# Performance work log

Hardware: AMD Instinct MI355X
Metric: run time of the kernel (lower is better)

Reference implementation:

```python
import jax, jax.numpy as jnp
import numpy as np

SLOPE = 10.0
NTR = 4.0
DTR = 0.0
DELTA = 3
MARG = 2


def _gt(x):
    return jax.nn.sigmoid(x * SLOPE)


def setup_inputs() -> dict:
    key = jax.random.key(0)
    x = jax.random.uniform(key, (16, 3, 512, 512), dtype=jnp.float32)
    return {"x": x}


def reference(x):
    B, C, H, W = x.shape
    d = DELTA
    # zero-pad H and W by delta (matches the two torch.cat calls)
    im_b = jnp.pad(x, ((0, 0), (0, 0), (d, d), (d, d)))

    roll_hw = lambda s: jnp.roll(im_b, s, axis=(2, 3))
    diff_11 = roll_hw((1, 1)) - im_b
    diff_nn11 = roll_hw((-1, -1)) - im_b
    diff_01 = roll_hw((0, 1)) - im_b
    diff_n01 = roll_hw((0, -1)) - im_b
    diff_10 = roll_hw((1, 0)) - im_b
    diff_n10 = roll_hw((-1, 0)) - im_b
    diff_n11 = roll_hw((-1, 1)) - im_b
    diff_1n1 = roll_hw((1, -1)) - im_b

    # NOTE: the original rolls the diff tensors over dims (1,2) = (channel, H).
    # We reproduce that exactly for faithfulness.
    rl = lambda t, s: jnp.roll(t, s, axis=(1, 2))

    ad_10 = jnp.abs(diff_10)
    ad_10 = ad_10 * _gt(ad_10 - DTR)
    e10a = _gt(ad_10 - jnp.abs(diff_01)) + _gt(ad_10 - jnp.abs(diff_n01)) + _gt(ad_10 - jnp.abs(diff_n10))
    # original repeats the roll(diff_01) term twice
    e10b = (_gt(ad_10 - jnp.abs(rl(diff_01, (1, 0))))
            + _gt(ad_10 - jnp.abs(rl(diff_n01, (1, 0))))
            + _gt(ad_10 - jnp.abs(rl(diff_01, (1, 0)))))
    g10 = _gt(e10a + e10b - NTR)
    e10 = g10 * _gt(diff_10)
    e10n = g10 * _gt(-diff_10)

    ad_01 = jnp.abs(diff_01)
    ad_01 = ad_01 * _gt(ad_10 - DTR)  # original uses ad_10 here (faithful)
    e01a = _gt(ad_01 - jnp.abs(diff_10)) + _gt(ad_01 - jnp.abs(diff_n10)) + _gt(ad_01 - jnp.abs(diff_n01))
    e01b = (_gt(ad_01 - jnp.abs(rl(diff_10, (0, 1))))
            + _gt(ad_01 - jnp.abs(rl(diff_n10, (0, 1))))
            + _gt(ad_01 - jnp.abs(rl(diff_01, (0, 1)))))
    g01 = _gt(e01a + e01b - NTR)
    e01 = g01 * _gt(diff_01)
    e01n = g01 * _gt(diff_01)  # original uses +diff_01 for both (faithful)

    ad_11 = jnp.abs(diff_11)
    ad_11 = ad_11 * _gt(ad_11 - DTR)
    e11a = _gt(ad_11 - jnp.abs(diff_n11)) + _gt(ad_11 - jnp.abs(diff_1n1)) + _gt(ad_11 - jnp.abs(diff_nn11))
    e11b = (_gt(ad_11 - jnp.abs(rl(diff_n11, (1, 1))))
            + _gt(ad_11 - jnp.abs(rl(diff_1n1, (1, 1))))
            + _gt(ad_11 - jnp.abs(rl(diff_11, (1, 1)))))
    g11 = _gt(e11a + e11b - NTR)
    e11 = g11 * _gt(diff_11)
    e11n = g11 * _gt(-diff_11)

    ad_n11 = jnp.abs(diff_n11)
    ad_n11 = ad_n11 * (ad_n11 > DTR).astype(x.dtype)  # hard threshold here (faithful)
    en11a = _gt(ad_n11 - jnp.abs(diff_11)) + _gt(ad_n11 - jnp.abs(diff_1n1)) + _gt(ad_n11 - jnp.abs(diff_nn11))
    en11b = (_gt(ad_n11 - jnp.abs(rl(diff_11, (-1, 1))))
             + _gt(ad_n11 - jnp.abs(rl(diff_n11, (-1, 1))))
             + _gt(ad_n11 - jnp.abs(rl(diff_n11, (-1, 1)))))
    gn11 = _gt(en11a + en11b - NTR)
    en11 = gn11 * _gt(diff_n11)
    en11n = gn11 * _gt(-diff_n11)

    def crop_pad(e):
        # interior crop back to HxW minus margins, zeros elsewhere
        c = e[:, :, d + MARG:d + H - MARG, d + MARG:d + W - MARG]
        return jnp.pad(c, ((0, 0), (0, 0), (MARG, MARG), (MARG, MARG)))

    edges = jnp.stack([crop_pad(e) for e in (e10, e10n, e01, e01n, e11, e11n, en11, en11n)], axis=2)
    # (B, C, 8, H, W) -> (B, 8*C, H, W) in torch's reshape order (C-major)
    return edges.reshape(B, C * 8, H, W)
```

## Files before the change

kernel.cpp:

```cpp
#include <hip/hip_runtime.h>

#define HH 512
#define WW 512
#define MARG 2

__device__ __forceinline__ float sigm(float t) {
    float e = __builtin_amdgcn_exp2f(t * -14.426950408889634f);
    return __builtin_amdgcn_rcpf(1.0f + e);
}

__global__ __launch_bounds__(256) void edge_kernel(const float* __restrict__ x,
                                                   float* __restrict__ out) {
    const int w = blockIdx.x * 64 + (threadIdx.x & 63);
    const int h = blockIdx.y * 4 + (threadIdx.x >> 6);
    const int b = blockIdx.z;

    const bool interior = (h >= MARG) & (h < HH - MARG) & (w >= MARG) & (w < WW - MARG);

    if (!interior) {
        const int base = ((b * 24) * HH + h) * WW + w;
        #pragma unroll
        for (int k = 0; k < 24; ++k) out[base + k * (HH * WW)] = 0.0f;
        return;
    }

    float X[3][4][3];
    #pragma unroll
    for (int j = 0; j < 3; ++j) {
        const float* p = x + ((size_t)(b * 3 + j) * HH + (h - 2)) * WW + (w - 1);
        #pragma unroll
        for (int r = 0; r < 4; ++r)
            #pragma unroll
            for (int q = 0; q < 3; ++q)
                X[j][r][q] = p[r * WW + q];
    }

    float A01[3], An01[3], rA11[3], rAn11[3], rA1n1[3];
    #pragma unroll
    for (int j = 0; j < 3; ++j) {
        const float v = X[j][2][1], u = X[j][1][1];
        A01[j]   = fabsf(X[j][2][0] - v);
        An01[j]  = fabsf(X[j][2][2] - v);
        rA11[j]  = fabsf(X[j][0][0] - u);
        rAn11[j] = fabsf(X[j][2][0] - u);
        rA1n1[j] = fabsf(X[j][0][2] - u);
    }

    #pragma unroll
    for (int c = 0; c < 3; ++c) {
        const int cm = (c + 2) % 3, cp = (c + 1) % 3;
        const float v = X[c][2][1], u = X[c][1][1];

        const float d10   = u            - v;
        const float dn10  = X[c][3][1]   - v;
        const float d01   = X[c][2][0]   - v;
        const float dn01  = X[c][2][2]   - v;
        const float d11   = X[c][1][0]   - v;
        const float dnn11 = X[c][3][2]   - v;
        const float dn11  = X[c][3][0]   - v;
        const float d1n1  = X[c][1][2]   - v;
        const float r_d10 = X[c][0][1]   - u;
        const float r_d01 = X[c][1][0]   - u;

        const int obase = ((b * 24 + c * 8) * HH + h) * WW + w;
        const int plane = HH * WW;

        const float a10  = fabsf(d10);
        const float ad10 = a10 * sigm(a10);
        const float e10s = sigm(ad10 - fabsf(d01)) + sigm(ad10 - fabsf(dn01)) + sigm(ad10 - fabsf(dn10))
                         + 2.0f * sigm(ad10 - A01[cm])
                         + sigm(ad10 - An01[cm]);
        const float g10 = sigm(e10s - 4.0f);
        const float s10 = sigm(d10);
        out[obase + 0 * plane] = g10 * s10;
        out[obase + 1 * plane] = g10 * (1.0f - s10);

        const float ad01 = fabsf(d01) * sigm(ad10);
        const float e01s = sigm(ad01 - a10) + sigm(ad01 - fabsf(dn10)) + sigm(ad01 - fabsf(dn01))
                         + sigm(ad01 - fabsf(r_d10)) + sigm(ad01 - a10) + sigm(ad01 - fabsf(r_d01));
        const float g01 = sigm(e01s - 4.0f);
        const float e01 = g01 * sigm(d01);
        out[obase + 2 * plane] = e01;
        out[obase + 3 * plane] = e01;

        const float a11  = fabsf(d11);
        const float ad11 = a11 * sigm(a11);
        const float e11s = sigm(ad11 - fabsf(dn11)) + sigm(ad11 - fabsf(d1n1)) + sigm(ad11 - fabsf(dnn11))
                         + sigm(ad11 - rAn11[cm]) + sigm(ad11 - rA1n1[cm]) + sigm(ad11 - rA11[cm]);
        const float g11 = sigm(e11s - 4.0f);
        const float s11 = sigm(d11);
        out[obase + 4 * plane] = g11 * s11;
        out[obase + 5 * plane] = g11 * (1.0f - s11);

        const float adn11 = fabsf(dn11);
        const float en11s = sigm(adn11 - a11) + sigm(adn11 - fabsf(d1n1)) + sigm(adn11 - fabsf(dnn11))
                          + sigm(adn11 - rA11[cp])
                          + 2.0f * sigm(adn11 - rAn11[cp]);
        const float gn11 = sigm(en11s - 4.0f);
        const float sn11 = sigm(dn11);
        out[obase + 6 * plane] = gn11 * sn11;
        out[obase + 7 * plane] = gn11 * (1.0f - sn11);
    }
}

extern "C" void kernel_launch(void* const* d_in, const int* in_sizes, int n_in,
                              void* d_out, int out_size, void* d_ws, size_t ws_size,
                              hipStream_t stream) {
    const float* x = (const float*)d_in[0];
    float* out = (float*)d_out;
    dim3 grid(WW / 64, HH / 4, 16);
    dim3 block(256);
    edge_kernel<<<grid, block, 0, stream>>>(x, out);
}
```

Before: 480.6 us.

## Process four columns per thread with float4 loads and stores

Each thread now computes four adjacent output columns. It loads a 6-wide window per row, with float4 for the centre four, and writes each of the 24 output planes as a float4. Column-margin handling moves from an early-exit branch to a multiplicative mask, and the grid shrinks fourfold. The aim is fewer, wider memory transactions and less redundant neighbour loading on this store-bound kernel. In exchange, per-thread register use rises and the total thread count falls, which may reduce occupancy.

```diff
diff --git a/kernel.cpp b/kernel.cpp
--- a/kernel.cpp
+++ b/kernel.cpp
@@ -2,7 +2,6 @@
 
 #define HH 512
 #define WW 512
-#define MARG 2
 
 __device__ __forceinline__ float sigm(float t) {
     float e = __builtin_amdgcn_exp2f(t * -14.426950408889634f);
@@ -11,95 +10,111 @@
 
 __global__ __launch_bounds__(256) void edge_kernel(const float* __restrict__ x,
                                                    float* __restrict__ out) {
-    const int w = blockIdx.x * 64 + (threadIdx.x & 63);
-    const int h = blockIdx.y * 4 + (threadIdx.x >> 6);
-    const int b = blockIdx.z;
+    const int tx = threadIdx.x & 63;
+    const int ty = threadIdx.x >> 6;
+    const int w0 = blockIdx.x * 256 + tx * 4;
+    const int h  = blockIdx.y * 4 + ty;
+    const int b  = blockIdx.z;
 
-    const bool interior = (h >= MARG) & (h < HH - MARG) & (w >= MARG) & (w < WW - MARG);
+    float4* outp = (float4*)(out + (((size_t)(b * 24) * HH + h) * WW + w0));
+    const int PL = HH * WW / 4;
 
-    if (!interior) {
-        const int base = ((b * 24) * HH + h) * WW + w;
+    if (h < 2 || h >= HH - 2) {
+        const float4 z = make_float4(0.f, 0.f, 0.f, 0.f);
         #pragma unroll
-        for (int k = 0; k < 24; ++k) out[base + k * (HH * WW)] = 0.0f;
+        for (int k = 0; k < 24; ++k) outp[k * PL] = z;
         return;
     }
 
-    float X[3][4][3];
+    float W6[3][4][6];
+    const int wl = (w0 == 0) ? 0 : (w0 - 1);
+    const int wr = (w0 + 4 >= WW) ? (WW - 1) : (w0 + 4);
     #pragma unroll
     for (int j = 0; j < 3; ++j) {
-        const float* p = x + ((size_t)(b * 3 + j) * HH + (h - 2)) * WW + (w - 1);
+        const float* rp = x + (((size_t)(b * 3 + j) * HH + (h - 2)) * WW);
         #pragma unroll
-        for (int r = 0; r < 4; ++r)
-            #pragma unroll
-            for (int q = 0; q < 3; ++q)
-                X[j][r][q] = p[r * WW + q];
-    }
-
-    float A01[3], An01[3], rA11[3], rAn11[3], rA1n1[3];
-    #pragma unroll
-    for (int j = 0; j < 3; ++j) {
-        const float v = X[j][2][1], u = X[j][1][1];
-        A01[j]   = fabsf(X[j][2][0] - v);
-        An01[j]  = fabsf(X[j][2][2] - v);
-        rA11[j]  = fabsf(X[j][0][0] - u);
-        rAn11[j] = fabsf(X[j][2][0] - u);
-        rA1n1[j] = fabsf(X[j][0][2] - u);
+        for (int r = 0; r < 4; ++r) {
+            const float* row = rp + r * WW;
+            const float4 m = *(const float4*)(row + w0);
+            W6[j][r][0] = row[wl];
+            W6[j][r][1] = m.x; W6[j][r][2] = m.y;
+            W6[j][r][3] = m.z; W6[j][r][4] = m.w;
+            W6[j][r][5] = row[wr];
+        }
     }
 
     #pragma unroll
     for (int c = 0; c < 3; ++c) {
         const int cm = (c + 2) % 3, cp = (c + 1) % 3;
-        const float v = X[c][2][1], u = X[c][1][1];
+        float acc[8][4];
+        #pragma unroll
+        for (int q = 0; q < 4; ++q) {
+            const float v = W6[c][2][q + 1], u = W6[c][1][q + 1];
+            const float d10   = u              - v;
+            const float dn10  = W6[c][3][q+1]  - v;
+            const float d01   = W6[c][2][q]    - v;
+            const float dn01  = W6[c][2][q+2]  - v;
+            const float d11   = W6[c][1][q]    - v;
+            const float dnn11 = W6[c][3][q+2]  - v;
+            const float dn11  = W6[c][3][q]    - v;
+            const float d1n1  = W6[c][1][q+2]  - v;
+            const float r_d10 = W6[c][0][q+1]  - u;
+            const float r_d01 = W6[c][1][q]    - u;
 
-        const float d10   = u            - v;
-        const float dn10  = X[c][3][1]   - v;
-        const float d01   = X[c][2][0]   - v;
-        const float dn01  = X[c][2][2]   - v;
-        const float d11   = X[c][1][0]   - v;
-        const float dnn11 = X[c][3][2]   - v;
-        const float dn11  = X[c][3][0]   - v;
-        const float d1n1  = X[c][1][2]   - v;
-        const float r_d10 = X[c][0][1]   - u;
-        const float r_d01 = X[c][1][0]   - u;
+            const float A01m   = fabsf(W6[cm][2][q]   - W6[cm][2][q+1]);
+            const float An01m  = fabsf(W6[cm][2][q+2] - W6[cm][2][q+1]);
+            const float rA11m  = fabsf(W6[cm][0][q]   - W6[cm][1][q+1]);
+            const float rAn11m = fabsf(W6[cm][2][q]   - W6[cm][1][q+1]);
+            const float rA1n1m = fabsf(W6[cm][0][q+2] - W6[cm][1][q+1]);
+            const float rA11p  = fabsf(W6[cp][0][q]   - W6[cp][1][q+1]);
+            const float rAn11p = fabsf(W6[cp][2][q]   - W6[cp][1][q+1]);
 
-        const int obase = ((b * 24 + c * 8) * HH + h) * WW + w;
-        const int plane = HH * WW;
+            const float msk = ((w0 + q) >= 2 && (w0 + q) < WW - 2) ? 1.0f : 0.0f;
 
-        const float a10  = fabsf(d10);
-        const float ad10 = a10 * sigm(a10);
-        const float e10s = sigm(ad10 - fabsf(d01)) + sigm(ad10 - fabsf(dn01)) + sigm(ad10 - fabsf(dn10))
-                         + 2.0f * sigm(ad10 - A01[cm])
-                         + sigm(ad10 - An01[cm]);
-        const float g10 = sigm(e10s - 4.0f);
-        const float s10 = sigm(d10);
-        out[obase + 0 * plane] = g10 * s10;
-        out[obase + 1 * plane] = g10 * (1.0f - s10);
+            const float a10  = fabsf(d10);
+            const float ad10 = a10 * sigm(a10);
+            const float e10s = sigm(ad10 - fabsf(d01)) + sigm(ad10 - fabsf(dn01))
+                             + sigm(ad10 - fabsf(dn10))
+                             + 2.0f * sigm(ad10 - A01m)
+                             + sigm(ad10 - An01m);
+            const float g10 = msk * sigm(e10s - 4.0f);
+            const float s10 = sigm(d10);
+            acc[0][q] = g10 * s10;
+            acc[1][q] = g10 * (1.0f - s10);
 
-        const float ad01 = fabsf(d01) * sigm(ad10);
-        const float e01s = sigm(ad01 - a10) + sigm(ad01 - fabsf(dn10)) + sigm(ad01 - fabsf(dn01))
-                         + sigm(ad01 - fabsf(r_d10)) + sigm(ad01 - a10) + sigm(ad01 - fabsf(r_d01));
-        const float g01 = sigm(e01s - 4.0f);
-        const float e01 = g01 * sigm(d01);
-        out[obase + 2 * plane] = e01;
-        out[obase + 3 * plane] = e01;
+            const float ad01 = fabsf(d01) * sigm(ad10);
+            const float e01s = 2.0f * sigm(ad01 - a10)
+                             + sigm(ad01 - fabsf(dn10)) + sigm(ad01 - fabsf(dn01))
+                             + sigm(ad01 - fabsf(r_d10)) + sigm(ad01 - fabsf(r_d01));
+            const float g01 = msk * sigm(e01s - 4.0f);
+            const float e01 = g01 * sigm(d01);
+            acc[2][q] = e01;
+            acc[3][q] = e01;
 
-        const float a11  = fabsf(d11);
-        const float ad11 = a11 * sigm(a11);
-        const float e11s = sigm(ad11 - fabsf(dn11)) + sigm(ad11 - fabsf(d1n1)) + sigm(ad11 - fabsf(dnn11))
-                         + sigm(ad11 - rAn11[cm]) + sigm(ad11 - rA1n1[cm]) + sigm(ad11 - rA11[cm]);
-        const float g11 = sigm(e11s - 4.0f);
-        const float s11 = sigm(d11);
-        out[obase + 4 * plane] = g11 * s11;
-        out[obase + 5 * plane] = g11 * (1.0f - s11);
+            const float a11  = fabsf(d11);
+            const float ad11 = a11 * sigm(a11);
+            const float e11s = sigm(ad11 - fabsf(dn11)) + sigm(ad11 - fabsf(d1n1))
+                             + sigm(ad11 - fabsf(dnn11))
+                             + sigm(ad11 - rAn11m) + sigm(ad11 - rA1n1m)
+                             + sigm(ad11 - rA11m);
+            const float g11 = msk * sigm(e11s - 4.0f);
+            const float s11 = sigm(d11);
+            acc[4][q] = g11 * s11;
+            acc[5][q] = g11 * (1.0f - s11);
 
-        const float adn11 = fabsf(dn11);
-        const float en11s = sigm(adn11 - a11) + sigm(adn11 - fabsf(d1n1)) + sigm(adn11 - fabsf(dnn11))
-                          + sigm(adn11 - rA11[cp])
-                          + 2.0f * sigm(adn11 - rAn11[cp]);
-        const float gn11 = sigm(en11s - 4.0f);
-        const float sn11 = sigm(dn11);
-        out[obase + 6 * plane] = gn11 * sn11;
-        out[obase + 7 * plane] = gn11 * (1.0f - sn11);
+            const float adn11 = fabsf(dn11);
+            const float en11s = sigm(adn11 - a11) + sigm(adn11 - fabsf(d1n1))
+                              + sigm(adn11 - fabsf(dnn11))
+                              + sigm(adn11 - rA11p)
+                              + 2.0f * sigm(adn11 - rAn11p);
+            const float gn11 = msk * sigm(en11s - 4.0f);
+            const float sn11 = sigm(dn11);
+            acc[6][q] = gn11 * sn11;
+            acc[7][q] = gn11 * (1.0f - sn11);
+        }
+        #pragma unroll
+        for (int k = 0; k < 8; ++k)
+            outp[(c * 8 + k) * PL] = make_float4(acc[k][0], acc[k][1], acc[k][2], acc[k][3]);
     }
 }
 
@@ -108,7 +123,7 @@
                               hipStream_t stream) {
     const float* x = (const float*)d_in[0];
     float* out = (float*)d_out;
-    dim3 grid(WW / 64, HH / 4, 16);
+    dim3 grid(WW / 256, HH / 4, 16);
     dim3 block(256);
     edge_kernel<<<grid, block, 0, stream>>>(x, out);
 }
```

Result: faster. 454.0 us (-5.5%).
